# Performance work log

Hardware: AMD Instinct MI355X
Metric: run time of the kernel (lower is better)

Reference implementation:

```python
import jax, jax.numpy as jnp
import numpy as np

E = 8          # num_global_experts (experts['count_per_node'])
D = 1024       # model_dim
H = 2048       # expert hidden_size
TOP_K = 2      # gate_type['k']


def setup_inputs() -> dict:
    key = jax.random.key(0)
    k_x, k_g, k_w1, k_w2 = jax.random.split(key, 4)
    B, S = 4, 2048
    inp = {
        "input": jax.random.normal(k_x, (B, S, D), dtype=jnp.float32),
        "Wg": jax.random.normal(k_g, (D, E), dtype=jnp.float32) * 0.02,
        "W1": jax.random.normal(k_w1, (E, D, H), dtype=jnp.float32) * 0.02,
        "b1": jnp.zeros((E, H), dtype=jnp.float32),
        "W2": jax.random.normal(k_w2, (E, H, D), dtype=jnp.float32) * 0.02,
        "b2": jnp.zeros((E, D), dtype=jnp.float32),
    }
    return inp


def reference(input, Wg, W1, b1, W2, b2):
    # ---- router: top-k softmax gating, gate weights normalized over top-k ----
    logits = jnp.einsum("bsd,de->bse", input, Wg)            # [B,S,E]
    probs = jax.nn.softmax(logits, axis=-1)                   # [B,S,E]
    top_vals, top_idx = jax.lax.top_k(probs, TOP_K)           # [B,S,K]
    top_vals = top_vals / jnp.sum(top_vals, axis=-1, keepdims=True)
    onehot = jax.nn.one_hot(top_idx, E, dtype=input.dtype)    # [B,S,K,E]
    mask = jnp.sum(onehot, axis=2)                            # [B,S,E] 0/1 dispatch mask (indices)
    scores = jnp.sum(onehot * top_vals[..., None], axis=2)    # [B,S,E] combine weights

    # ---- dense masked dispatch: repeat input per expert, mask non-routed tokens ----
    xm = input[None] * jnp.moveaxis(mask, -1, 0)[..., None]   # [E,B,S,D]

    # ---- per-expert 2-layer MLP (LinearExperts) ----
    h = jnp.einsum("ebsd,edh->ebsh", xm, W1) + b1[:, None, None, :]
    h = jax.nn.relu(h)                                        # [E,B,S,H]
    y = jnp.einsum("ebsh,ehd->ebsd", h, W2) + b2[:, None, None, :]

    # ---- weighted combine: sum_e expert_out * gate score ----
    out = jnp.sum(y * jnp.moveaxis(scores, -1, 0)[..., None], axis=0)  # [B,S,D]
    return out
```

## Files before the change

### kernel.cpp

```cpp
#include <hip/hip_runtime.h>
#include <hip/hip_bf16.h>

typedef __bf16 bf16x8 __attribute__((ext_vector_type(8)));
typedef __bf16 bf16x4 __attribute__((ext_vector_type(4)));
typedef float  f32x4  __attribute__((ext_vector_type(4)));

#define T_TOK    8192
#define D_DIM    1024
#define H_DIM    2048
#define E_NUM    8
#define MAX_MB   136
#define MAX_ROWS 17408

#define OFF_MBTOT   512
#define OFF_MB2E    1024
#define OFF_MBROW0  2048
#define OFF_TOPKE   4096
#define OFF_TOPKS   69632
#define OFF_TOK     135168
#define OFF_ROWIDX  204800
#define OFF_XB      (1u<<20)
#define OFF_W1T     (18u*1024*1024)
#define OFF_W2T     (50u*1024*1024)
#define OFF_HBUF    (82u*1024*1024)
#define OFF_YBUF    OFF_XB

__device__ __forceinline__ void gload_lds16(const void* g, void* l) {
    __builtin_amdgcn_global_load_lds(
        (const __attribute__((address_space(1))) void*)g,
        (__attribute__((address_space(3))) void*)l, 16, 0, 0);
}

__global__ __launch_bounds__(256) void k_router_cvt(
    const float* __restrict__ x, const float* __restrict__ Wg,
    __bf16* __restrict__ xb, int* __restrict__ topk_e, float* __restrict__ topk_s)
{
    __shared__ float wgT[E_NUM][1032];
    const int tid = threadIdx.x;
#pragma unroll
    for (int i = 0; i < 32; ++i) {
        int f = tid + i * 256;
        wgT[f & 7][f >> 3] = Wg[f];
    }
    __syncthreads();

    const int wave = tid >> 6, lane = tid & 63;
    const int t = blockIdx.x * 4 + wave;
    const float* xr = x + (size_t)t * D_DIM;
    __bf16* xbr = xb + (size_t)t * D_DIM;

    float acc[E_NUM];
#pragma unroll
    for (int e = 0; e < E_NUM; ++e) acc[e] = 0.f;

#pragma unroll
    for (int j = 0; j < 4; ++j) {
        const int d0 = lane * 4 + j * 256;
        float4 xv = *(const float4*)(xr + d0);
        bf16x4 o = { (__bf16)xv.x, (__bf16)xv.y, (__bf16)xv.z, (__bf16)xv.w };
        *(bf16x4*)(xbr + d0) = o;
#pragma unroll
        for (int e = 0; e < E_NUM; ++e) {
            float4 wv = *(const float4*)&wgT[e][d0];
            acc[e] += xv.x * wv.x + xv.y * wv.y + xv.z * wv.z + xv.w * wv.w;
        }
    }
#pragma unroll
    for (int off = 32; off >= 1; off >>= 1)
#pragma unroll
        for (int e = 0; e < E_NUM; ++e) acc[e] += __shfl_xor(acc[e], off, 64);

    if (lane == 0) {
        int e0 = 0; float v0 = acc[0];
#pragma unroll
        for (int e = 1; e < E_NUM; ++e) if (acc[e] > v0) { v0 = acc[e]; e0 = e; }
        int e1 = -1; float v1 = -1e30f;
#pragma unroll
        for (int e = 0; e < E_NUM; ++e) if (e != e0 && acc[e] > v1) { v1 = acc[e]; e1 = e; }
        float s0 = 1.f / (1.f + __expf(v1 - v0));
        float s1 = 1.f - s0;
        topk_e[t*2+0] = e0; topk_e[t*2+1] = e1;
        topk_s[t*2+0] = s0; topk_s[t*2+1] = s1;
    }
}

#define SORT_T 256
__global__ __launch_bounds__(512) void k_sort(
    const int* __restrict__ topk_e,
    int* __restrict__ mbTot, int* __restrict__ mb2e, int* __restrict__ mbrow0,
    int* __restrict__ tok, int* __restrict__ rowidx)
{
    __shared__ int lcnt[E_NUM][SORT_T];
    __shared__ int base[E_NUM];
    __shared__ int etot[E_NUM];
    const int tid = threadIdx.x;

    if (tid < SORT_T) {
#pragma unroll
        for (int e = 0; e < E_NUM; ++e) lcnt[e][tid] = 0;
    }
    __syncthreads();

    if (tid < SORT_T) {
        const int4* p = (const int4*)(topk_e + tid * 64);
#pragma unroll
        for (int i = 0; i < 16; ++i) {
            int4 v = p[i];
            lcnt[v.x][tid]++; lcnt[v.y][tid]++; lcnt[v.z][tid]++; lcnt[v.w][tid]++;
        }
    }
    __syncthreads();

    {
        const int w = tid >> 6, l = tid & 63;
        int v0 = lcnt[w][l*4+0], v1 = lcnt[w][l*4+1], v2 = lcnt[w][l*4+2], v3 = lcnt[w][l*4+3];
        int s = v0 + v1 + v2 + v3;
        int inc = s;
#pragma unroll
        for (int off = 1; off < 64; off <<= 1) {
            int o = __shfl_up(inc, off, 64);
            if (l >= off) inc += o;
        }
        int exc = inc - s;
        lcnt[w][l*4+0] = exc;
        lcnt[w][l*4+1] = exc + v0;
        lcnt[w][l*4+2] = exc + v0 + v1;
        lcnt[w][l*4+3] = exc + v0 + v1 + v2;
        if (l == 63) etot[w] = inc;
    }
    __syncthreads();

    if (tid == 0) {
        int row = 0, mb = 0;
        for (int e = 0; e < E_NUM; ++e) {
            base[e] = row;
            int nb = (etot[e] + 127) >> 7;
            for (int b = 0; b < nb; ++b) { mb2e[mb] = e; mbrow0[mb] = row + b*128; ++mb; }
            row += nb * 128;
        }
        mbTot[0] = mb;
    }
    __syncthreads();

    if (tid < SORT_T) {
#pragma unroll
        for (int e = 0; e < E_NUM; ++e) lcnt[e][tid] += base[e];
        const int4* p = (const int4*)(topk_e + tid * 64);
#pragma unroll
        for (int i = 0; i < 16; ++i) {
            int4 v = p[i];
            int j0 = tid * 64 + i * 4;
            int r;
            r = lcnt[v.x][tid]++; tok[r] = (j0+0) >> 1; rowidx[j0+0] = r;
            r = lcnt[v.y][tid]++; tok[r] = (j0+1) >> 1; rowidx[j0+1] = r;
            r = lcnt[v.z][tid]++; tok[r] = (j0+2) >> 1; rowidx[j0+2] = r;
            r = lcnt[v.w][tid]++; tok[r] = (j0+3) >> 1; rowidx[j0+3] = r;
        }
    }
}

__global__ __launch_bounds__(256) void k_transpose(
    const float* __restrict__ in, __bf16* __restrict__ out, int R, int C)
{
    __shared__ float tile[64][65];
    const int e = blockIdx.z;
    const float* inp = in + (size_t)e * R * C;
    __bf16* outp = out + (size_t)e * R * C;
    const int r0 = blockIdx.x * 64, c0 = blockIdx.y * 64;
    const int c = threadIdx.x & 63, rr = threadIdx.x >> 6;
#pragma unroll
    for (int i = 0; i < 16; ++i) {
        int r = rr + i * 4;
        tile[r][c] = inp[(size_t)(r0 + r) * C + c0 + c];
    }
    __syncthreads();
#pragma unroll
    for (int i = 0; i < 16; ++i) {
        int cc = rr + i * 4;
        outp[(size_t)(c0 + cc) * R + r0 + c] = (__bf16)tile[c][cc];
    }
}

__global__ __launch_bounds__(256) void k_gemm1(
    const __bf16* __restrict__ xb, const __bf16* __restrict__ W1T,
    const float* __restrict__ b1, const int* __restrict__ tok,
    const int* __restrict__ mb2e, const int* __restrict__ mbrow0,
    const int* __restrict__ mbTot, __bf16* __restrict__ hbuf)
{
    const int id   = blockIdx.x;
    const int xcd  = id & 7;
    const int j    = id >> 3;
    const int nblk = j & 15;
    const int mb   = (j >> 4) * 8 + xcd;
    if (mb >= *mbTot) return;
    const int e    = mb2e[mb];
    const int row0 = mbrow0[mb];
    const int n0   = nblk * 128;

    __shared__ __align__(16) char smem[16384];

    const int tid = threadIdx.x;
    const int w = tid >> 6, l = tid & 63;
    const int part = (l & 3) ^ ((l >> 3) & 3);

    const __bf16* Wb = W1T + (size_t)e * (size_t)(H_DIM * D_DIM);
    const __bf16* gA[2]; const __bf16* gB[2];
#pragma unroll
    for (int jj = 0; jj < 2; ++jj) {
        int rr = (w*2 + jj) * 16 + (l >> 2);
        int t  = tok[row0 + rr];
        gA[jj] = xb + (size_t)t * D_DIM + part * 8;
        gB[jj] = Wb + (size_t)(n0 + rr) * D_DIM + part * 8;
    }
    char* ldsA0 = smem + (w*2 + 0) * 1024;
    char* ldsA1 = smem + (w*2 + 1) * 1024;
    char* ldsB0 = smem + 8192 + (w*2 + 0) * 1024;
    char* ldsB1 = smem + 8192 + (w*2 + 1) * 1024;

    const int r = l & 15, q = l >> 4;
    const int wm = w & 1, wn = w >> 1;
    const int qx = (q ^ ((r >> 1) & 3)) * 16;

    f32x4 acc[4][4];
#pragma unroll
    for (int mi = 0; mi < 4; ++mi)
#pragma unroll
        for (int ni = 0; ni < 4; ++ni) acc[mi][ni] = (f32x4){0.f, 0.f, 0.f, 0.f};

    for (int k0 = 0; k0 < D_DIM; k0 += 32) {
        gload_lds16(gA[0] + k0, ldsA0);
        gload_lds16(gA[1] + k0, ldsA1);
        gload_lds16(gB[0] + k0, ldsB0);
        gload_lds16(gB[1] + k0, ldsB1);
        __syncthreads();

        bf16x8 av[4], bv[4];
#pragma unroll
        for (int mi = 0; mi < 4; ++mi)
            av[mi] = *(const bf16x8*)(smem + ((wm*64 + mi*16 + r) * 64 + qx));
#pragma unroll
        for (int ni = 0; ni < 4; ++ni)
            bv[ni] = *(const bf16x8*)(smem + 8192 + ((wn*64 + ni*16 + r) * 64 + qx));
#pragma unroll
        for (int mi = 0; mi < 4; ++mi)
#pragma unroll
            for (int ni = 0; ni < 4; ++ni)
                acc[mi][ni] = __builtin_amdgcn_mfma_f32_16x16x32_bf16(av[mi], bv[ni], acc[mi][ni], 0, 0, 0);
        __syncthreads();
    }

    const float* b1e = b1 + (size_t)e * H_DIM;
    float bb[4];
#pragma unroll
    for (int ni = 0; ni < 4; ++ni) bb[ni] = b1e[n0 + wn*64 + ni*16 + r];
#pragma unroll
    for (int mi = 0; mi < 4; ++mi)
#pragma unroll
        for (int reg = 0; reg < 4; ++reg) {
            int m = wm*64 + mi*16 + q*4 + reg;
            __bf16* hrow = hbuf + (size_t)(row0 + m) * H_DIM + n0 + wn*64;
#pragma unroll
            for (int ni = 0; ni < 4; ++ni) {
                float v = acc[mi][ni][reg] + bb[ni];
                hrow[ni*16 + r] = (__bf16)fmaxf(v, 0.f);
            }
        }
}

__global__ __launch_bounds__(256) void k_gemm2(
    const __bf16* __restrict__ hbuf, const __bf16* __restrict__ W2T,
    const float* __restrict__ b2, const int* __restrict__ mb2e,
    const int* __restrict__ mbrow0, const int* __restrict__ mbTot,
    __bf16* __restrict__ ybuf)
{
    const int id   = blockIdx.x;
    const int xcd  = id & 7;
    const int j    = id >> 3;
    const int nblk = j & 7;
    const int mb   = (j >> 3) * 8 + xcd;
    if (mb >= *mbTot) return;
    const int e    = mb2e[mb];
    const int row0 = mbrow0[mb];
    const int n0   = nblk * 128;

    __shared__ __align__(16) char smem[16384];

    const int tid = threadIdx.x;
    const int w = tid >> 6, l = tid & 63;
    const int part = (l & 3) ^ ((l >> 3) & 3);

    const __bf16* Wb = W2T + (size_t)e * (size_t)(D_DIM * H_DIM);
    const __bf16* gA[2]; const __bf16* gB[2];
#pragma unroll
    for (int jj = 0; jj < 2; ++jj) {
        int rr = (w*2 + jj) * 16 + (l >> 2);
        gA[jj] = hbuf + (size_t)(row0 + rr) * H_DIM + part * 8;
        gB[jj] = Wb + (size_t)(n0 + rr) * H_DIM + part * 8;
    }
    char* ldsA0 = smem + (w*2 + 0) * 1024;
    char* ldsA1 = smem + (w*2 + 1) * 1024;
    char* ldsB0 = smem + 8192 + (w*2 + 0) * 1024;
    char* ldsB1 = smem + 8192 + (w*2 + 1) * 1024;

    const int r = l & 15, q = l >> 4;
    const int wm = w & 1, wn = w >> 1;
    const int qx = (q ^ ((r >> 1) & 3)) * 16;

    f32x4 acc[4][4];
#pragma unroll
    for (int mi = 0; mi < 4; ++mi)
#pragma unroll
        for (int ni = 0; ni < 4; ++ni) acc[mi][ni] = (f32x4){0.f, 0.f, 0.f, 0.f};

    for (int k0 = 0; k0 < H_DIM; k0 += 32) {
        gload_lds16(gA[0] + k0, ldsA0);
        gload_lds16(gA[1] + k0, ldsA1);
        gload_lds16(gB[0] + k0, ldsB0);
        gload_lds16(gB[1] + k0, ldsB1);
        __syncthreads();

        bf16x8 av[4], bv[4];
#pragma unroll
        for (int mi = 0; mi < 4; ++mi)
            av[mi] = *(const bf16x8*)(smem + ((wm*64 + mi*16 + r) * 64 + qx));
#pragma unroll
        for (int ni = 0; ni < 4; ++ni)
            bv[ni] = *(const bf16x8*)(smem + 8192 + ((wn*64 + ni*16 + r) * 64 + qx));
#pragma unroll
        for (int mi = 0; mi < 4; ++mi)
#pragma unroll
            for (int ni = 0; ni < 4; ++ni)
                acc[mi][ni] = __builtin_amdgcn_mfma_f32_16x16x32_bf16(av[mi], bv[ni], acc[mi][ni], 0, 0, 0);
        __syncthreads();
    }

    const float* b2e = b2 + (size_t)e * D_DIM;
    float bb[4];
#pragma unroll
    for (int ni = 0; ni < 4; ++ni) bb[ni] = b2e[n0 + wn*64 + ni*16 + r];
#pragma unroll
    for (int mi = 0; mi < 4; ++mi)
#pragma unroll
        for (int reg = 0; reg < 4; ++reg) {
            int row = row0 + wm*64 + mi*16 + q*4 + reg;
            __bf16* yrow = ybuf + (size_t)row * D_DIM + n0 + wn*64;
#pragma unroll
            for (int ni = 0; ni < 4; ++ni)
                yrow[ni*16 + r] = (__bf16)(acc[mi][ni][reg] + bb[ni]);
        }
}

__global__ __launch_bounds__(256) void k_combine(
    const __bf16* __restrict__ ybuf, const int* __restrict__ rowidx,
    const float* __restrict__ topk_s, float* __restrict__ out)
{
    const int t = blockIdx.x;
    const int d0 = threadIdx.x * 4;
    const int r0 = rowidx[t*2+0], r1 = rowidx[t*2+1];
    const float s0 = topk_s[t*2+0], s1 = topk_s[t*2+1];
    bf16x4 y0 = *(const bf16x4*)(ybuf + (size_t)r0 * D_DIM + d0);
    bf16x4 y1 = *(const bf16x4*)(ybuf + (size_t)r1 * D_DIM + d0);
    float4 o;
    o.x = s0 * (float)y0[0] + s1 * (float)y1[0];
    o.y = s0 * (float)y0[1] + s1 * (float)y1[1];
    o.z = s0 * (float)y0[2] + s1 * (float)y1[2];
    o.w = s0 * (float)y0[3] + s1 * (float)y1[3];
    *(float4*)(out + (size_t)t * D_DIM + d0) = o;
}

extern "C" void kernel_launch(void* const* d_in, const int* in_sizes, int n_in,
                              void* d_out, int out_size, void* d_ws, size_t ws_size,
                              hipStream_t stream) {
    const float* x  = (const float*)d_in[0];
    const float* Wg = (const float*)d_in[1];
    const float* W1 = (const float*)d_in[2];
    const float* b1 = (const float*)d_in[3];
    const float* W2 = (const float*)d_in[4];
    const float* b2 = (const float*)d_in[5];
    float* out = (float*)d_out;
    char* ws = (char*)d_ws;

    int*   mbTot  = (int*)  (ws + OFF_MBTOT);
    int*   mb2e   = (int*)  (ws + OFF_MB2E);
    int*   mbrow0 = (int*)  (ws + OFF_MBROW0);
    int*   topk_e = (int*)  (ws + OFF_TOPKE);
    float* topk_s = (float*)(ws + OFF_TOPKS);
    int*   tok    = (int*)  (ws + OFF_TOK);
    int*   rowidx = (int*)  (ws + OFF_ROWIDX);
    __bf16* xb   = (__bf16*)(ws + OFF_XB);
    __bf16* W1T  = (__bf16*)(ws + OFF_W1T);
    __bf16* W2T  = (__bf16*)(ws + OFF_W2T);
    __bf16* hbuf = (__bf16*)(ws + OFF_HBUF);
    __bf16* ybuf = (__bf16*)(ws + OFF_YBUF);

    hipMemsetAsync(ws + OFF_TOK, 0, MAX_ROWS * sizeof(int), stream);

    k_router_cvt<<<T_TOK/4, 256, 0, stream>>>(x, Wg, xb, topk_e, topk_s);
    k_sort      <<<1, 512, 0, stream>>>(topk_e, mbTot, mb2e, mbrow0, tok, rowidx);
    k_transpose <<<dim3(D_DIM/64, H_DIM/64, E_NUM), 256, 0, stream>>>(W1, W1T, D_DIM, H_DIM);
    k_transpose <<<dim3(H_DIM/64, D_DIM/64, E_NUM), 256, 0, stream>>>(W2, W2T, H_DIM, D_DIM);

    k_gemm1<<<MAX_MB * (H_DIM/128), 256, 0, stream>>>(xb, W1T, b1, tok, mb2e, mbrow0, mbTot, hbuf);
    k_gemm2<<<MAX_MB * (D_DIM/128), 256, 0, stream>>>(hbuf, W2T, b2, mb2e, mbrow0, mbTot, ybuf);
    k_combine<<<T_TOK, 256, 0, stream>>>(ybuf, rowidx, topk_s, out);
}
```

Measured before the change: 430.7 us.

## Double GEMM K-tile to 64 with XOR-swizzled LDS; read router weights from global

Both expert GEMM kernels now stage a 64-wide K slice per iteration (32KB LDS) instead of 32, with a new 8-chunk XOR swizzle for the direct global-to-LDS loads and matching reads. This halves the number of barrier pairs per K loop and gives each stage two MFMA sub-steps to amortize load latency. The router kernel drops its per-block LDS transpose of Wg and reads Wg rows directly from global/cache, removing a sync and shared-memory setup. The larger LDS footprint may lower occupancy.

```diff
diff --git a/kernel.cpp b/kernel.cpp
--- a/kernel.cpp
+++ b/kernel.cpp
@@ -35,15 +35,7 @@
     const float* __restrict__ x, const float* __restrict__ Wg,
     __bf16* __restrict__ xb, int* __restrict__ topk_e, float* __restrict__ topk_s)
 {
-    __shared__ float wgT[E_NUM][1032];
     const int tid = threadIdx.x;
-#pragma unroll
-    for (int i = 0; i < 32; ++i) {
-        int f = tid + i * 256;
-        wgT[f & 7][f >> 3] = Wg[f];
-    }
-    __syncthreads();
-
     const int wave = tid >> 6, lane = tid & 63;
     const int t = blockIdx.x * 4 + wave;
     const float* xr = x + (size_t)t * D_DIM;
@@ -59,10 +51,16 @@
         float4 xv = *(const float4*)(xr + d0);
         bf16x4 o = { (__bf16)xv.x, (__bf16)xv.y, (__bf16)xv.z, (__bf16)xv.w };
         *(bf16x4*)(xbr + d0) = o;
-#pragma unroll
-        for (int e = 0; e < E_NUM; ++e) {
-            float4 wv = *(const float4*)&wgT[e][d0];
-            acc[e] += xv.x * wv.x + xv.y * wv.y + xv.z * wv.z + xv.w * wv.w;
+        const float* xvf = (const float*)&xv;
+#pragma unroll
+        for (int u = 0; u < 4; ++u) {
+            float4 wlo = *(const float4*)(Wg + (size_t)(d0 + u) * E_NUM);
+            float4 whi = *(const float4*)(Wg + (size_t)(d0 + u) * E_NUM + 4);
+            float xd = xvf[u];
+            acc[0] += xd * wlo.x; acc[1] += xd * wlo.y;
+            acc[2] += xd * wlo.z; acc[3] += xd * wlo.w;
+            acc[4] += xd * whi.x; acc[5] += xd * whi.y;
+            acc[6] += xd * whi.z; acc[7] += xd * whi.w;
         }
     }
 #pragma unroll
@@ -180,6 +178,7 @@
         outp[(size_t)(c0 + cc) * R + r0 + c] = (__bf16)tile[c][cc];
     }
 }
+
 
 __global__ __launch_bounds__(256) void k_gemm1(
     const __bf16* __restrict__ xb, const __bf16* __restrict__ W1T,
@@ -197,29 +196,27 @@
     const int row0 = mbrow0[mb];
     const int n0   = nblk * 128;
 
-    __shared__ __align__(16) char smem[16384];
+    __shared__ __align__(16) char smem[32768];
 
     const int tid = threadIdx.x;
     const int w = tid >> 6, l = tid & 63;
-    const int part = (l & 3) ^ ((l >> 3) & 3);
+    const int lrow  = l >> 3;
+    const int chunk = (l & 7) ^ lrow;
 
     const __bf16* Wb = W1T + (size_t)e * (size_t)(H_DIM * D_DIM);
-    const __bf16* gA[2]; const __bf16* gB[2];
-#pragma unroll
-    for (int jj = 0; jj < 2; ++jj) {
-        int rr = (w*2 + jj) * 16 + (l >> 2);
-        int t  = tok[row0 + rr];
-        gA[jj] = xb + (size_t)t * D_DIM + part * 8;
-        gB[jj] = Wb + (size_t)(n0 + rr) * D_DIM + part * 8;
-    }
-    char* ldsA0 = smem + (w*2 + 0) * 1024;
-    char* ldsA1 = smem + (w*2 + 1) * 1024;
-    char* ldsB0 = smem + 8192 + (w*2 + 0) * 1024;
-    char* ldsB1 = smem + 8192 + (w*2 + 1) * 1024;
+    const __bf16* gA[4]; const __bf16* gB[4];
+#pragma unroll
+    for (int jj = 0; jj < 4; ++jj) {
+        int rr = w*32 + jj*8 + lrow;
+        gA[jj] = xb + (size_t)tok[row0 + rr] * D_DIM + chunk * 8;
+        gB[jj] = Wb + (size_t)(n0 + rr) * D_DIM + chunk * 8;
+    }
+    char* ldsA = smem + w*4096 + l*16;
+    char* ldsB = smem + 16384 + w*4096 + l*16;
 
     const int r = l & 15, q = l >> 4;
     const int wm = w & 1, wn = w >> 1;
-    const int qx = (q ^ ((r >> 1) & 3)) * 16;
+    const int r7 = r & 7;
 
     f32x4 acc[4][4];
 #pragma unroll
@@ -227,25 +224,29 @@
 #pragma unroll
         for (int ni = 0; ni < 4; ++ni) acc[mi][ni] = (f32x4){0.f, 0.f, 0.f, 0.f};
 
-    for (int k0 = 0; k0 < D_DIM; k0 += 32) {
-        gload_lds16(gA[0] + k0, ldsA0);
-        gload_lds16(gA[1] + k0, ldsA1);
-        gload_lds16(gB[0] + k0, ldsB0);
-        gload_lds16(gB[1] + k0, ldsB1);
+    for (int k0 = 0; k0 < D_DIM; k0 += 64) {
+#pragma unroll
+        for (int jj = 0; jj < 4; ++jj) gload_lds16(gA[jj] + k0, ldsA + jj*1024);
+#pragma unroll
+        for (int jj = 0; jj < 4; ++jj) gload_lds16(gB[jj] + k0, ldsB + jj*1024);
         __syncthreads();
 
-        bf16x8 av[4], bv[4];
-#pragma unroll
-        for (int mi = 0; mi < 4; ++mi)
-            av[mi] = *(const bf16x8*)(smem + ((wm*64 + mi*16 + r) * 64 + qx));
-#pragma unroll
-        for (int ni = 0; ni < 4; ++ni)
-            bv[ni] = *(const bf16x8*)(smem + 8192 + ((wn*64 + ni*16 + r) * 64 + qx));
-#pragma unroll
-        for (int mi = 0; mi < 4; ++mi)
+#pragma unroll
+        for (int s = 0; s < 2; ++s) {
+            const int cx = ((s*4 + q) ^ r7) * 16;
+            bf16x8 av[4], bv[4];
+#pragma unroll
+            for (int mi = 0; mi < 4; ++mi)
+                av[mi] = *(const bf16x8*)(smem + (wm*64 + mi*16 + r) * 128 + cx);
 #pragma unroll
             for (int ni = 0; ni < 4; ++ni)
-                acc[mi][ni] = __builtin_amdgcn_mfma_f32_16x16x32_bf16(av[mi], bv[ni], acc[mi][ni], 0, 0, 0);
+                bv[ni] = *(const bf16x8*)(smem + 16384 + (wn*64 + ni*16 + r) * 128 + cx);
+#pragma unroll
+            for (int mi = 0; mi < 4; ++mi)
+#pragma unroll
+                for (int ni = 0; ni < 4; ++ni)
+                    acc[mi][ni] = __builtin_amdgcn_mfma_f32_16x16x32_bf16(av[mi], bv[ni], acc[mi][ni], 0, 0, 0);
+        }
         __syncthreads();
     }
 
@@ -283,28 +284,27 @@
     const int row0 = mbrow0[mb];
     const int n0   = nblk * 128;
 
-    __shared__ __align__(16) char smem[16384];
+    __shared__ __align__(16) char smem[32768];
 
     const int tid = threadIdx.x;
     const int w = tid >> 6, l = tid & 63;
-    const int part = (l & 3) ^ ((l >> 3) & 3);
+    const int lrow  = l >> 3;
+    const int chunk = (l & 7) ^ lrow;
 
     const __bf16* Wb = W2T + (size_t)e * (size_t)(D_DIM * H_DIM);
-    const __bf16* gA[2]; const __bf16* gB[2];
-#pragma unroll
-    for (int jj = 0; jj < 2; ++jj) {
-        int rr = (w*2 + jj) * 16 + (l >> 2);
-        gA[jj] = hbuf + (size_t)(row0 + rr) * H_DIM + part * 8;
-        gB[jj] = Wb + (size_t)(n0 + rr) * H_DIM + part * 8;
-    }
-    char* ldsA0 = smem + (w*2 + 0) * 1024;
-    char* ldsA1 = smem + (w*2 + 1) * 1024;
-    char* ldsB0 = smem + 8192 + (w*2 + 0) * 1024;
-    char* ldsB1 = smem + 8192 + (w*2 + 1) * 1024;
+    const __bf16* gA[4]; const __bf16* gB[4];
+#pragma unroll
+    for (int jj = 0; jj < 4; ++jj) {
+        int rr = w*32 + jj*8 + lrow;
+        gA[jj] = hbuf + (size_t)(row0 + rr) * H_DIM + chunk * 8;
+        gB[jj] = Wb + (size_t)(n0 + rr) * H_DIM + chunk * 8;
+    }
+    char* ldsA = smem + w*4096 + l*16;
+    char* ldsB = smem + 16384 + w*4096 + l*16;
 
     const int r = l & 15, q = l >> 4;
     const int wm = w & 1, wn = w >> 1;
-    const int qx = (q ^ ((r >> 1) & 3)) * 16;
+    const int r7 = r & 7;
 
     f32x4 acc[4][4];
 #pragma unroll
@@ -312,25 +312,29 @@
 #pragma unroll
         for (int ni = 0; ni < 4; ++ni) acc[mi][ni] = (f32x4){0.f, 0.f, 0.f, 0.f};
 
-    for (int k0 = 0; k0 < H_DIM; k0 += 32) {
-        gload_lds16(gA[0] + k0, ldsA0);
-        gload_lds16(gA[1] + k0, ldsA1);
-        gload_lds16(gB[0] + k0, ldsB0);
-        gload_lds16(gB[1] + k0, ldsB1);
+    for (int k0 = 0; k0 < H_DIM; k0 += 64) {
+#pragma unroll
+        for (int jj = 0; jj < 4; ++jj) gload_lds16(gA[jj] + k0, ldsA + jj*1024);
+#pragma unroll
+        for (int jj = 0; jj < 4; ++jj) gload_lds16(gB[jj] + k0, ldsB + jj*1024);
         __syncthreads();
 
-        bf16x8 av[4], bv[4];
-#pragma unroll
-        for (int mi = 0; mi < 4; ++mi)
-            av[mi] = *(const bf16x8*)(smem + ((wm*64 + mi*16 + r) * 64 + qx));
-#pragma unroll
-        for (int ni = 0; ni < 4; ++ni)
-            bv[ni] = *(const bf16x8*)(smem + 8192 + ((wn*64 + ni*16 + r) * 64 + qx));
-#pragma unroll
-        for (int mi = 0; mi < 4; ++mi)
+#pragma unroll
+        for (int s = 0; s < 2; ++s) {
+            const int cx = ((s*4 + q) ^ r7) * 16;
+            bf16x8 av[4], bv[4];
+#pragma unroll
+            for (int mi = 0; mi < 4; ++mi)
+                av[mi] = *(const bf16x8*)(smem + (wm*64 + mi*16 + r) * 128 + cx);
 #pragma unroll
             for (int ni = 0; ni < 4; ++ni)
-                acc[mi][ni] = __builtin_amdgcn_mfma_f32_16x16x32_bf16(av[mi], bv[ni], acc[mi][ni], 0, 0, 0);
+                bv[ni] = *(const bf16x8*)(smem + 16384 + (wn*64 + ni*16 + r) * 128 + cx);
+#pragma unroll
+            for (int mi = 0; mi < 4; ++mi)
+#pragma unroll
+                for (int ni = 0; ni < 4; ++ni)
+                    acc[mi][ni] = __builtin_amdgcn_mfma_f32_16x16x32_bf16(av[mi], bv[ni], acc[mi][ni], 0, 0, 0);
+        }
         __syncthreads();
     }
 
```

After: 452.8 us. 1.05x slower.
